# Performance work log

Measured on AMD Instinct MI355X. Metric: run time of the kernel, lower is better.

The kernel has to match this reference:

```python
import jax, jax.numpy as jnp
import numpy as np

DIM = 1024
N_HEADS = 16
HEAD_DIM = DIM // N_HEADS
SCALE = 1.0 / HEAD_DIM ** 0.5


def setup_inputs() -> dict:
    key = jax.random.key(0)
    k1, k2, k3, k4, k5 = jax.random.split(key, 5)
    B, T = 4, 2048
    x = jax.random.normal(k1, (B, T, DIM), dtype=jnp.float32)
    # torch nn.Linear weights: y = x @ W.T + b
    w_qkv = jax.random.normal(k2, (3 * DIM, DIM), dtype=jnp.float32) * 0.02
    b_qkv = jax.random.normal(k3, (3 * DIM,), dtype=jnp.float32) * 0.02
    w_proj = jax.random.normal(k4, (DIM, DIM), dtype=jnp.float32) * 0.02
    b_proj = jax.random.normal(k5, (DIM,), dtype=jnp.float32) * 0.02
    return {"x": x, "w_qkv": w_qkv, "b_qkv": b_qkv, "w_proj": w_proj, "b_proj": b_proj}


def reference(x, w_qkv, b_qkv, w_proj, b_proj):
    B, T, D = x.shape
    qkv = x @ w_qkv.T + b_qkv                              # [B, T, 3D]
    qkv = qkv.reshape(B, T, 3, N_HEADS, HEAD_DIM)
    qkv = jnp.transpose(qkv, (2, 0, 3, 1, 4))              # [3, B, h, T, d]
    q, k, v = qkv[0], qkv[1], qkv[2]
    s = jnp.einsum('bhqd,bhkd->bhqk', q, k) * SCALE        # [B, h, T, T]
    attn = jax.nn.softmax(s, axis=-1)
    out = jnp.einsum('bhqk,bhkd->bqhd', attn, v)           # [B, T, h, d]
    out = out.reshape(B, T, D)
    return out @ w_proj.T + b_proj
```

## Files before the change

kernel.cpp:

```cpp
#include <hip/hip_runtime.h>
#include <stdint.h>

typedef short short8 __attribute__((ext_vector_type(8)));
typedef _Float16 half4 __attribute__((ext_vector_type(4)));
typedef __fp16 fp16x2 __attribute__((ext_vector_type(2)));
typedef unsigned int uint2v __attribute__((ext_vector_type(2)));
typedef float floatx4 __attribute__((ext_vector_type(4)));

#define LOG2E 1.44269504088896340736f
#define QSCALE (0.125f * LOG2E)

static __device__ __forceinline__ unsigned short f2bf(float f) {
  unsigned int u = __float_as_uint(f);
  u += 0x7fffu + ((u >> 16) & 1u);
  return (unsigned short)(u >> 16);
}

static __device__ __forceinline__ float fexp2(float x) {
#if __has_builtin(__builtin_amdgcn_exp2f)
  return __builtin_amdgcn_exp2f(x);
#else
  return exp2f(x);
#endif
}

#define GLD_LDS16(gp, lp)                                                      \
  __builtin_amdgcn_global_load_lds(                                            \
      (const __attribute__((address_space(1))) void*)(gp),                     \
      (__attribute__((address_space(3))) void*)(lp), 16, 0, 0)

__global__ __launch_bounds__(256) void cvt_f32_bf16(
    const float* __restrict__ in, unsigned short* __restrict__ out, int n) {
  int i = (blockIdx.x * 256 + threadIdx.x) * 4;
  if (i >= n) return;
  float4 v = *(const float4*)(in + i);
  ushort4 u;
  u.x = f2bf(v.x); u.y = f2bf(v.y); u.z = f2bf(v.z); u.w = f2bf(v.w);
  *(ushort4*)(out + i) = u;
}

template <int MODE>
__global__ __launch_bounds__(256, 2) void gemm_bt(
    const unsigned short* __restrict__ A, const unsigned short* __restrict__ Bm,
    const float* __restrict__ bias, float* __restrict__ outF,
    unsigned short* __restrict__ qo, unsigned short* __restrict__ ko,
    _Float16* __restrict__ vto, int M, int N, int K) {
  __shared__ unsigned short As[128 * 64];
  __shared__ unsigned short Bs[128 * 64];
  const int tid = threadIdx.x;
  const int w = tid >> 6, l = tid & 63;
  const int lr = l & 15, lg = l >> 4;
  const int nbn = N >> 7;
  const int nwg = gridDim.x;
  const int bid = blockIdx.x;
  const int cpx = nwg >> 3;
  const int swz = (bid & 7) * cpx + (bid >> 3);
  const int bm = swz / nbn, bn = swz % nbn;
  const int wm = w >> 1, wn = w & 1;

  floatx4 acc[4][4];
#pragma unroll
  for (int i = 0; i < 4; ++i)
#pragma unroll
    for (int j = 0; j < 4; ++j) acc[i][j] = (floatx4){0.f, 0.f, 0.f, 0.f};

  for (int k0 = 0; k0 < K; k0 += 64) {
#pragma unroll
    for (int i = 0; i < 4; ++i) {
      int c = i * 256 + tid;
      const unsigned short* ga =
          A + ((size_t)bm * 128 + (c >> 3)) * K + k0 + (c & 7) * 8;
      GLD_LDS16(ga, As + (size_t)(i * 256 + w * 64) * 8);
    }
#pragma unroll
    for (int i = 0; i < 4; ++i) {
      int c = i * 256 + tid;
      const unsigned short* gb =
          Bm + ((size_t)bn * 128 + (c >> 3)) * K + k0 + (c & 7) * 8;
      GLD_LDS16(gb, Bs + (size_t)(i * 256 + w * 64) * 8);
    }
    __syncthreads();
#pragma unroll
    for (int kk = 0; kk < 2; ++kk) {
      short8 af[4], bf[4];
#pragma unroll
      for (int i = 0; i < 4; ++i)
        af[i] = *(const short8*)&As[(wm * 64 + i * 16 + lr) * 64 + kk * 32 + lg * 8];
#pragma unroll
      for (int j = 0; j < 4; ++j)
        bf[j] = *(const short8*)&Bs[(wn * 64 + j * 16 + lr) * 64 + kk * 32 + lg * 8];
#pragma unroll
      for (int i = 0; i < 4; ++i)
#pragma unroll
        for (int j = 0; j < 4; ++j)
          acc[i][j] = __builtin_amdgcn_mfma_f32_16x16x32_bf16(af[i], bf[j],
                                                              acc[i][j], 0, 0, 0);
    }
    __syncthreads();
  }

#pragma unroll
  for (int i = 0; i < 4; ++i) {
    int row0 = bm * 128 + wm * 64 + i * 16 + lg * 4;
#pragma unroll
    for (int j = 0; j < 4; ++j) {
      int col = bn * 128 + wn * 64 + j * 16 + lr;
      float bv = bias[col];
#pragma unroll
      for (int jj = 0; jj < 4; ++jj) {
        float v = acc[i][j][jj] + bv;
        int r = row0 + jj;
        if (MODE == 0) {
          outF[(size_t)r * N + col] = v;
        } else {
          int three = col >> 10, cc = col & 1023;
          int h = cc >> 6, d = cc & 63;
          int b = r >> 11, t = r & 2047;
          if (three == 0)
            qo[(((size_t)(b * 16 + h)) * 2048 + t) * 64 + d] = f2bf(v * QSCALE);
          else if (three == 1)
            ko[(((size_t)(b * 16 + h)) * 2048 + t) * 64 + d] = f2bf(v);
          else
            vto[(((size_t)(b * 16 + h)) * 64 + d) * 2048 + t] = (_Float16)v;
        }
      }
    }
  }
}

__global__ __launch_bounds__(256, 3) void attn_fwd(
    const unsigned short* __restrict__ Qg, const unsigned short* __restrict__ Kg,
    const _Float16* __restrict__ VTg, unsigned short* __restrict__ Og) {
  __shared__ unsigned short Ks[2][64 * 64];
  __shared__ _Float16 Vs[2][64 * 64];

  const int bid0 = blockIdx.x;
  const int bid = (bid0 & 7) * 128 + (bid0 >> 3);
  const int bh = bid >> 4, qt = bid & 15;
  const int b = bh >> 4, hh = bh & 15;
  const int tid = threadIdx.x, w = tid >> 6, l = tid & 63;
  const int l4 = l & 15, g = l >> 4;
  const unsigned short* Q = Qg + (size_t)bh * (2048 * 64);
  const unsigned short* Kp = Kg + (size_t)bh * (2048 * 64);
  const _Float16* VT = VTg + (size_t)bh * (64 * 2048);
  const int qw = qt * 128 + w * 32;

#define STAGE(bufidx, tt)                                                     \
  do {                                                                        \
    int c0 = tid, c1 = 256 + tid;                                             \
    int r0 = c0 >> 3, s0 = (c0 & 7) ^ (r0 & 7);                               \
    int r1 = c1 >> 3, s1 = (c1 & 7) ^ (r1 & 7);                               \
    GLD_LDS16(Kp + (size_t)((tt) + r0) * 64 + s0 * 8, &Ks[bufidx][c0 * 8]);   \
    GLD_LDS16(Kp + (size_t)((tt) + r1) * 64 + s1 * 8, &Ks[bufidx][c1 * 8]);   \
    GLD_LDS16(VT + (size_t)r0 * 2048 + (tt) + s0 * 8, &Vs[bufidx][c0 * 8]);   \
    GLD_LDS16(VT + (size_t)r1 * 2048 + (tt) + s1 * 8, &Vs[bufidx][c1 * 8]);   \
  } while (0)

  short8 qf[2][2];
#pragma unroll
  for (int qs = 0; qs < 2; ++qs)
#pragma unroll
    for (int c = 0; c < 2; ++c)
      qf[qs][c] =
          *(const short8*)&Q[(size_t)(qw + qs * 16 + l4) * 64 + c * 32 + g * 8];

  floatx4 o[2][4];
#pragma unroll
  for (int qs = 0; qs < 2; ++qs)
#pragma unroll
    for (int db = 0; db < 4; ++db) o[qs][db] = (floatx4){0.f, 0.f, 0.f, 0.f};
  float m[2] = {-__builtin_inff(), -__builtin_inff()};
  float lp[2] = {0.f, 0.f};

  STAGE(0, 0);
  __syncthreads();

  for (int it = 0; it < 32; ++it) {
    const int cur = it & 1;
    if (it + 1 < 32) STAGE(cur ^ 1, (it + 1) * 64);

    floatx4 s[2][4];
#pragma unroll
    for (int f = 0; f < 4; ++f) {
      short8 kf0 = *(const short8*)&Ks[cur][(f * 16 + l4) * 64 +
                                            ((g ^ (l4 & 7)) * 8)];
      short8 kf1 = *(const short8*)&Ks[cur][(f * 16 + l4) * 64 +
                                            (((4 + g) ^ (l4 & 7)) * 8)];
      floatx4 z = (floatx4){0.f, 0.f, 0.f, 0.f};
      floatx4 t00 = __builtin_amdgcn_mfma_f32_16x16x32_bf16(kf0, qf[0][0], z, 0, 0, 0);
      s[0][f] = __builtin_amdgcn_mfma_f32_16x16x32_bf16(kf1, qf[0][1], t00, 0, 0, 0);
      floatx4 t10 = __builtin_amdgcn_mfma_f32_16x16x32_bf16(kf0, qf[1][0], z, 0, 0, 0);
      s[1][f] = __builtin_amdgcn_mfma_f32_16x16x32_bf16(kf1, qf[1][1], t10, 0, 0, 0);
    }

    half4 pf[2][4];
#pragma unroll
    for (int qs = 0; qs < 2; ++qs) {
      float a0 = fmaxf(fmaxf(s[qs][0][0], s[qs][0][1]), fmaxf(s[qs][0][2], s[qs][0][3]));
      float a1 = fmaxf(fmaxf(s[qs][1][0], s[qs][1][1]), fmaxf(s[qs][1][2], s[qs][1][3]));
      float a2 = fmaxf(fmaxf(s[qs][2][0], s[qs][2][1]), fmaxf(s[qs][2][2], s[qs][2][3]));
      float a3 = fmaxf(fmaxf(s[qs][3][0], s[qs][3][1]), fmaxf(s[qs][3][2], s[qs][3][3]));
      float pp = fmaxf(fmaxf(a0, a1), fmaxf(a2, a3));

      if (!__all(pp - m[qs] <= 8.0f)) {
        float pmf = fmaxf(pp, __shfl_xor(pp, 16));
        pmf = fmaxf(pmf, __shfl_xor(pmf, 32));
        float mo = m[qs];
        m[qs] = fmaxf(mo, pmf);
        float al = fexp2(mo - m[qs]);
        lp[qs] *= al;
#pragma unroll
        for (int jj = 0; jj < 4; ++jj) {
          float alr = __shfl(al, g * 4 + jj);
          o[qs][0][jj] *= alr; o[qs][1][jj] *= alr;
          o[qs][2][jj] *= alr; o[qs][3][jj] *= alr;
        }
      }

      float rs = 0.f;
#pragma unroll
      for (int f = 0; f < 4; ++f) {
        float p0 = fexp2(s[qs][f][0] - m[qs]), p1 = fexp2(s[qs][f][1] - m[qs]);
        float p2 = fexp2(s[qs][f][2] - m[qs]), p3 = fexp2(s[qs][f][3] - m[qs]);
        rs += (p0 + p1) + (p2 + p3);
        fp16x2 plo = __builtin_amdgcn_cvt_pkrtz(p0, p1);
        fp16x2 phi = __builtin_amdgcn_cvt_pkrtz(p2, p3);
        uint2v u;
        u.x = __builtin_bit_cast(unsigned int, plo);
        u.y = __builtin_bit_cast(unsigned int, phi);
        pf[qs][f] = __builtin_bit_cast(half4, u);
      }
      lp[qs] += rs;
    }

#pragma unroll
    for (int db = 0; db < 4; ++db) {
#pragma unroll
      for (int f = 0; f < 4; ++f) {
        half4 vf = *(const half4*)&Vs[cur][(db * 16 + l4) * 64 +
                                           (((2 * f + (g >> 1)) ^ (l4 & 7)) * 8 +
                                            (g & 1) * 4)];
        o[0][db] = __builtin_amdgcn_mfma_f32_16x16x16f16(pf[0][f], vf, o[0][db], 0, 0, 0);
        o[1][db] = __builtin_amdgcn_mfma_f32_16x16x16f16(pf[1][f], vf, o[1][db], 0, 0, 0);
      }
    }
    __syncthreads();
  }

#pragma unroll
  for (int qs = 0; qs < 2; ++qs) {
    float ls = lp[qs];
    ls += __shfl_xor(ls, 16);
    ls += __shfl_xor(ls, 32);
    float invq = 1.f / ls;
    float inv[4];
#pragma unroll
    for (int jj = 0; jj < 4; ++jj) inv[jj] = __shfl(invq, g * 4 + jj);
#pragma unroll
    for (int db = 0; db < 4; ++db)
#pragma unroll
      for (int jj = 0; jj < 4; ++jj)
        Og[((size_t)b * 2048 + qw + qs * 16 + g * 4 + jj) * 1024 + hh * 64 +
           db * 16 + l4] = f2bf(o[qs][db][jj] * inv[jj]);
  }
#undef STAGE
}

extern "C" void kernel_launch(void* const* d_in, const int* in_sizes, int n_in,
                              void* d_out, int out_size, void* d_ws, size_t ws_size,
                              hipStream_t stream) {
  const float* x = (const float*)d_in[0];
  const float* w_qkv = (const float*)d_in[1];
  const float* b_qkv = (const float*)d_in[2];
  const float* w_proj = (const float*)d_in[3];
  const float* b_proj = (const float*)d_in[4];
  float* out = (float*)d_out;

  char* p = (char*)d_ws;
  unsigned short* xb = (unsigned short*)p;     p += (size_t)8192 * 1024 * 2;
  unsigned short* wqkvb = (unsigned short*)p;  p += (size_t)3072 * 1024 * 2;
  unsigned short* wprojb = (unsigned short*)p; p += (size_t)1024 * 1024 * 2;
  unsigned short* qb = (unsigned short*)p;     p += (size_t)64 * 2048 * 64 * 2;
  unsigned short* kb = (unsigned short*)p;     p += (size_t)64 * 2048 * 64 * 2;
  _Float16* vtb = (_Float16*)p;                p += (size_t)64 * 64 * 2048 * 2;
  unsigned short* attnb = (unsigned short*)p;  p += (size_t)8192 * 1024 * 2;

  cvt_f32_bf16<<<dim3(8192), dim3(256), 0, stream>>>(x, xb, 8192 * 1024);
  cvt_f32_bf16<<<dim3(3072), dim3(256), 0, stream>>>(w_qkv, wqkvb, 3072 * 1024);
  cvt_f32_bf16<<<dim3(1024), dim3(256), 0, stream>>>(w_proj, wprojb, 1024 * 1024);

  gemm_bt<1><<<dim3(64 * 24), dim3(256), 0, stream>>>(
      xb, wqkvb, b_qkv, nullptr, qb, kb, vtb, 8192, 3072, 1024);

  attn_fwd<<<dim3(1024), dim3(256), 0, stream>>>(qb, kb, vtb, attnb);

  gemm_bt<0><<<dim3(64 * 8), dim3(256), 0, stream>>>(
      attnb, wprojb, b_proj, out, nullptr, nullptr, nullptr, 8192, 1024, 1024);
}
```

Before: 225.9 us.

## Compute exp first and rescale only when row sum overflows; hoist addresses

The softmax step now computes the exponentials against the stale running max first. It falls back to the max reduction and rescale only if any lane's partial sum exceeds a threshold, which removes the 16 fmax ops per row per iteration in the common case. Global-to-LDS staging addresses and LDS read offsets are precomputed outside the loop, and the KV loop is unrolled by two. The fallback path recomputes all exps, so frequent max growth costs extra, and the partial-sum check is a different overflow test than the original max-delta check.

```diff
diff --git a/kernel.cpp b/kernel.cpp
--- a/kernel.cpp
+++ b/kernel.cpp
@@ -145,16 +145,32 @@
   const _Float16* VT = VTg + (size_t)bh * (64 * 2048);
   const int qw = qt * 128 + w * 32;
 
-#define STAGE(bufidx, tt)                                                     \
+  const int c0 = tid, c1 = 256 + tid;
+  const int r0 = c0 >> 3, s0 = (c0 & 7) ^ (r0 & 7);
+  const int r1 = c1 >> 3, s1 = (c1 & 7) ^ (r1 & 7);
+  const unsigned short* kp0 = Kp + (size_t)r0 * 64 + s0 * 8;
+  const unsigned short* kp1 = Kp + (size_t)r1 * 64 + s1 * 8;
+  const _Float16* vp0 = VT + (size_t)r0 * 2048 + s0 * 8;
+  const _Float16* vp1 = VT + (size_t)r1 * 2048 + s1 * 8;
+  unsigned short* ksd0 = &Ks[0][c0 * 8];
+  unsigned short* ksd1 = &Ks[0][c1 * 8];
+  _Float16* vsd0 = &Vs[0][c0 * 8];
+  _Float16* vsd1 = &Vs[0][c1 * 8];
+
+#define STAGE(bufofs, tt)                                                     \
   do {                                                                        \
-    int c0 = tid, c1 = 256 + tid;                                             \
-    int r0 = c0 >> 3, s0 = (c0 & 7) ^ (r0 & 7);                               \
-    int r1 = c1 >> 3, s1 = (c1 & 7) ^ (r1 & 7);                               \
-    GLD_LDS16(Kp + (size_t)((tt) + r0) * 64 + s0 * 8, &Ks[bufidx][c0 * 8]);   \
-    GLD_LDS16(Kp + (size_t)((tt) + r1) * 64 + s1 * 8, &Ks[bufidx][c1 * 8]);   \
-    GLD_LDS16(VT + (size_t)r0 * 2048 + (tt) + s0 * 8, &Vs[bufidx][c0 * 8]);   \
-    GLD_LDS16(VT + (size_t)r1 * 2048 + (tt) + s1 * 8, &Vs[bufidx][c1 * 8]);   \
+    GLD_LDS16(kp0 + (size_t)(tt) * 64, ksd0 + (bufofs) * 4096);               \
+    GLD_LDS16(kp1 + (size_t)(tt) * 64, ksd1 + (bufofs) * 4096);               \
+    GLD_LDS16(vp0 + (tt), vsd0 + (bufofs) * 4096);                            \
+    GLD_LDS16(vp1 + (tt), vsd1 + (bufofs) * 4096);                            \
   } while (0)
+
+  const int kb0 = l4 * 64 + ((g ^ (l4 & 7)) * 8);
+  const int kb1 = l4 * 64 + (((4 + g) ^ (l4 & 7)) * 8);
+  int vb[4];
+#pragma unroll
+  for (int f = 0; f < 4; ++f)
+    vb[f] = l4 * 64 + (((2 * f + (g >> 1)) ^ (l4 & 7)) * 8 + (g & 1) * 4);
 
   short8 qf[2][2];
 #pragma unroll
@@ -175,6 +191,7 @@
   STAGE(0, 0);
   __syncthreads();
 
+#pragma unroll 2
   for (int it = 0; it < 32; ++it) {
     const int cur = it & 1;
     if (it + 1 < 32) STAGE(cur ^ 1, (it + 1) * 64);
@@ -182,10 +199,8 @@
     floatx4 s[2][4];
 #pragma unroll
     for (int f = 0; f < 4; ++f) {
-      short8 kf0 = *(const short8*)&Ks[cur][(f * 16 + l4) * 64 +
-                                            ((g ^ (l4 & 7)) * 8)];
-      short8 kf1 = *(const short8*)&Ks[cur][(f * 16 + l4) * 64 +
-                                            (((4 + g) ^ (l4 & 7)) * 8)];
+      short8 kf0 = *(const short8*)&Ks[cur][kb0 + f * 1024];
+      short8 kf1 = *(const short8*)&Ks[cur][kb1 + f * 1024];
       floatx4 z = (floatx4){0.f, 0.f, 0.f, 0.f};
       floatx4 t00 = __builtin_amdgcn_mfma_f32_16x16x32_bf16(kf0, qf[0][0], z, 0, 0, 0);
       s[0][f] = __builtin_amdgcn_mfma_f32_16x16x32_bf16(kf1, qf[0][1], t00, 0, 0, 0);
@@ -196,17 +211,27 @@
     half4 pf[2][4];
 #pragma unroll
     for (int qs = 0; qs < 2; ++qs) {
-      float a0 = fmaxf(fmaxf(s[qs][0][0], s[qs][0][1]), fmaxf(s[qs][0][2], s[qs][0][3]));
-      float a1 = fmaxf(fmaxf(s[qs][1][0], s[qs][1][1]), fmaxf(s[qs][1][2], s[qs][1][3]));
-      float a2 = fmaxf(fmaxf(s[qs][2][0], s[qs][2][1]), fmaxf(s[qs][2][2], s[qs][2][3]));
-      float a3 = fmaxf(fmaxf(s[qs][3][0], s[qs][3][1]), fmaxf(s[qs][3][2], s[qs][3][3]));
-      float pp = fmaxf(fmaxf(a0, a1), fmaxf(a2, a3));
-
-      if (!__all(pp - m[qs] <= 8.0f)) {
-        float pmf = fmaxf(pp, __shfl_xor(pp, 16));
-        pmf = fmaxf(pmf, __shfl_xor(pmf, 32));
+      float e[16];
+      float rs = 0.f;
+#pragma unroll
+      for (int f = 0; f < 4; ++f)
+#pragma unroll
+        for (int jj = 0; jj < 4; ++jj) {
+          float pv = fexp2(s[qs][f][jj] - m[qs]);
+          e[f * 4 + jj] = pv;
+          rs += pv;
+        }
+
+      if (!__all(rs <= 256.0f)) {
+        float a0 = fmaxf(fmaxf(s[qs][0][0], s[qs][0][1]), fmaxf(s[qs][0][2], s[qs][0][3]));
+        float a1 = fmaxf(fmaxf(s[qs][1][0], s[qs][1][1]), fmaxf(s[qs][1][2], s[qs][1][3]));
+        float a2 = fmaxf(fmaxf(s[qs][2][0], s[qs][2][1]), fmaxf(s[qs][2][2], s[qs][2][3]));
+        float a3 = fmaxf(fmaxf(s[qs][3][0], s[qs][3][1]), fmaxf(s[qs][3][2], s[qs][3][3]));
+        float pp = fmaxf(fmaxf(a0, a1), fmaxf(a2, a3));
+        pp = fmaxf(pp, __shfl_xor(pp, 16));
+        pp = fmaxf(pp, __shfl_xor(pp, 32));
         float mo = m[qs];
-        m[qs] = fmaxf(mo, pmf);
+        m[qs] = fmaxf(mo, pp);
         float al = fexp2(mo - m[qs]);
         lp[qs] *= al;
 #pragma unroll
@@ -215,31 +240,34 @@
           o[qs][0][jj] *= alr; o[qs][1][jj] *= alr;
           o[qs][2][jj] *= alr; o[qs][3][jj] *= alr;
         }
+        rs = 0.f;
+#pragma unroll
+        for (int f = 0; f < 4; ++f)
+#pragma unroll
+          for (int jj = 0; jj < 4; ++jj) {
+            float pv = fexp2(s[qs][f][jj] - m[qs]);
+            e[f * 4 + jj] = pv;
+            rs += pv;
+          }
       }
-
-      float rs = 0.f;
+      lp[qs] += rs;
+
 #pragma unroll
       for (int f = 0; f < 4; ++f) {
-        float p0 = fexp2(s[qs][f][0] - m[qs]), p1 = fexp2(s[qs][f][1] - m[qs]);
-        float p2 = fexp2(s[qs][f][2] - m[qs]), p3 = fexp2(s[qs][f][3] - m[qs]);
-        rs += (p0 + p1) + (p2 + p3);
-        fp16x2 plo = __builtin_amdgcn_cvt_pkrtz(p0, p1);
-        fp16x2 phi = __builtin_amdgcn_cvt_pkrtz(p2, p3);
+        fp16x2 plo = __builtin_amdgcn_cvt_pkrtz(e[f * 4 + 0], e[f * 4 + 1]);
+        fp16x2 phi = __builtin_amdgcn_cvt_pkrtz(e[f * 4 + 2], e[f * 4 + 3]);
         uint2v u;
         u.x = __builtin_bit_cast(unsigned int, plo);
         u.y = __builtin_bit_cast(unsigned int, phi);
         pf[qs][f] = __builtin_bit_cast(half4, u);
       }
-      lp[qs] += rs;
     }
 
 #pragma unroll
     for (int db = 0; db < 4; ++db) {
 #pragma unroll
       for (int f = 0; f < 4; ++f) {
-        half4 vf = *(const half4*)&Vs[cur][(db * 16 + l4) * 64 +
-                                           (((2 * f + (g >> 1)) ^ (l4 & 7)) * 8 +
-                                            (g & 1) * 4)];
+        half4 vf = *(const half4*)&Vs[cur][vb[f] + db * 1024];
         o[0][db] = __builtin_amdgcn_mfma_f32_16x16x16f16(pf[0][f], vf, o[0][db], 0, 0, 0);
         o[1][db] = __builtin_amdgcn_mfma_f32_16x16x16f16(pf[1][f], vf, o[1][db], 0, 0, 0);
       }
```

Result: faster. 217.8 us (-3.6%).
